# Kernel tuning notes

Hardware: AMD Instinct MI355X
Metric: run time of the kernel (lower is better)

The kernel has to match this reference:

```python
import jax, jax.numpy as jnp
import numpy as np

B, S, E, H, C = 32, 256, 768, 512, 30
IN0 = E + 2  # LSTM layer-0 input size (770)


def _lstm_dir(x_sbf, Wih, Whh, bih, bhh, reverse):
    """One LSTM direction. x_sbf: [S,B,F]. PyTorch gate order i,f,g,o. Returns [S,B,H]."""
    h0 = jnp.zeros((x_sbf.shape[1], Whh.shape[1]), x_sbf.dtype)
    c0 = jnp.zeros_like(h0)
    xW = jnp.einsum('sbf,gf->sbg', x_sbf, Wih) + (bih + bhh)  # precompute input proj

    def step(carry, xw_t):
        h, c = carry
        gates = xw_t + h @ Whh.T
        i, f, g, o = jnp.split(gates, 4, axis=-1)
        c = jax.nn.sigmoid(f) * c + jax.nn.sigmoid(i) * jnp.tanh(g)
        h = jax.nn.sigmoid(o) * jnp.tanh(c)
        return (h, c), h

    _, ys = jax.lax.scan(step, (h0, c0), xW, reverse=reverse)
    return ys  # aligned with input time order


def _bilstm_layer(x_sbf, Wf, Uf, bif, bhf, Wb, Ub, bib, bhb):
    hf = _lstm_dir(x_sbf, Wf, Uf, bif, bhf, reverse=False)
    hb = _lstm_dir(x_sbf, Wb, Ub, bib, bhb, reverse=True)
    return jnp.concatenate([hf, hb], axis=-1)  # [S,B,2H]


def setup_inputs() -> dict:
    key = jax.random.key(0)
    ks = jax.random.split(key, 24)
    d = {
        'hidden_states': jax.random.normal(ks[0], (4, B, S, E), jnp.float32),
        'roles': jax.random.randint(ks[1], (B, S), 0, C),
        'predicates': jax.random.randint(ks[2], (B, S), 0, 2),
    }
    G = 4 * H
    shapes = {
        'Wih_l0f': (G, IN0), 'Whh_l0f': (G, H), 'bih_l0f': (G,), 'bhh_l0f': (G,),
        'Wih_l0b': (G, IN0), 'Whh_l0b': (G, H), 'bih_l0b': (G,), 'bhh_l0b': (G,),
        'Wih_l1f': (G, 2 * H), 'Whh_l1f': (G, H), 'bih_l1f': (G,), 'bhh_l1f': (G,),
        'Wih_l1b': (G, 2 * H), 'Whh_l1b': (G, H), 'bih_l1b': (G,), 'bhh_l1b': (G,),
        'W_out': (C, 2 * H), 'b_out': (C,),
    }
    for i, (name, shp) in enumerate(shapes.items()):
        d[name] = jax.random.normal(ks[3 + i], shp, jnp.float32) * 0.05
    return d


def reference(hidden_states, roles, predicates,
              Wih_l0f, Whh_l0f, bih_l0f, bhh_l0f,
              Wih_l0b, Whh_l0b, bih_l0b, bhh_l0b,
              Wih_l1f, Whh_l1f, bih_l1f, bhh_l1f,
              Wih_l1b, Whh_l1b, bih_l1b, bhh_l1b,
              W_out, b_out):
    # mean of last-4 transformer hidden states: [B,S,E]
    out = hidden_states.mean(axis=0)
    # vectorized predicate-relative features (replaces the Python .item() loops)
    idx_pred = jnp.argmax(predicates, axis=-1)                      # [B]
    mean_word = out.mean(axis=-1)                                   # [B,S]
    mean_pred = jnp.take_along_axis(mean_word, idx_pred[:, None], axis=1)  # [B,1]
    delta = mean_word - mean_pred                                   # [B,S]
    role_mask = ((roles != 0) & (roles != -100)).astype(out.dtype)  # [B,S]
    x = jnp.concatenate([out, delta[..., None], role_mask[..., None]], axis=-1)  # [B,S,E+2]

    # 2-layer BiLSTM (eval mode; inter-layer dropout inactive)
    x = jnp.swapaxes(x, 0, 1)  # [S,B,F]
    x = _bilstm_layer(x, Wih_l0f, Whh_l0f, bih_l0f, bhh_l0f,
                      Wih_l0b, Whh_l0b, bih_l0b, bhh_l0b)
    x = _bilstm_layer(x, Wih_l1f, Whh_l1f, bih_l1f, bhh_l1f,
                      Wih_l1b, Whh_l1b, bih_l1b, bhh_l1b)
    x = jnp.swapaxes(x, 0, 1)  # [B,S,2H]
    return x @ W_out.T + b_out  # [B,S,classes]
```

## Files before the change

### kernel.cpp

```cpp
#include <hip/hip_runtime.h>
#include <hip/hip_bf16.h>
#include <math.h>

#define BB 32
#define SS 256
#define EE 768
#define HH 512
#define GG 2048
#define NCLS 30
#define NWG 16

typedef __attribute__((ext_vector_type(8))) short bf16x8;
typedef __attribute__((ext_vector_type(4))) float f32x4;
typedef unsigned long long u64;

__device__ inline unsigned short f2bf(float f) {
  union { float f; unsigned int u; } v; v.f = f;
  unsigned int r = v.u + 0x7fffu + ((v.u >> 16) & 1u);
  return (unsigned short)(r >> 16);
}
__device__ inline float bf2f(unsigned short u) {
  union { unsigned int u; float f; } v; v.u = ((unsigned int)u) << 16;
  return v.f;
}
__device__ inline float sigm(float x) { return 1.f / (1.f + expf(-x)); }

__device__ inline void load_lds16(const void* g, void* l) {
  __builtin_amdgcn_global_load_lds(
      (const __attribute__((address_space(1))) void*)g,
      (__attribute__((address_space(3))) void*)l, 16, 0, 0);
}

__device__ inline u64 aload64(const u64* p) {
  return __hip_atomic_load(p, __ATOMIC_RELAXED, __HIP_MEMORY_SCOPE_AGENT);
}
__device__ inline void astore64(u64* p, u64 v) {
  __hip_atomic_store(p, v, __ATOMIC_RELAXED, __HIP_MEMORY_SCOPE_AGENT);
}
__device__ inline int aload32(const int* p) {
  return __hip_atomic_load(p, __ATOMIC_RELAXED, __HIP_MEMORY_SCOPE_AGENT);
}
__device__ inline void astore32(int* p, int v) {
  __hip_atomic_store(p, v, __ATOMIC_RELAXED, __HIP_MEMORY_SCOPE_AGENT);
}
__device__ inline void wait_vm0() {
  asm volatile("s_waitcnt vmcnt(0)" ::: "memory");
}

__global__ void k_convpad(const float* __restrict__ src, unsigned short* __restrict__ dst,
                          int R, int Ks, int Kd) {
  int n = R * Kd;
  for (int i = blockIdx.x * blockDim.x + threadIdx.x; i < n; i += gridDim.x * blockDim.x) {
    int r = i / Kd, k = i - r * Kd;
    dst[i] = (k < Ks) ? f2bf(src[(size_t)r * Ks + k]) : (unsigned short)0;
  }
}

__global__ void k_biassum(const float* __restrict__ a, const float* __restrict__ b,
                          float* __restrict__ o) {
  int i = blockIdx.x * 256 + threadIdx.x;
  if (i < GG) o[i] = a[i] + b[i];
}

__global__ void k_meanword(const float* __restrict__ hs, float* __restrict__ mw) {
  int blk = blockIdx.x;
  int b = blk >> 8, s = blk & 255;
  __shared__ float red[256];
  size_t base = ((size_t)b * SS + s) * EE;
  const size_t LSTR = (size_t)BB * SS * EE;
  float acc = 0.f;
  for (int l = 0; l < 4; l++)
    for (int e = threadIdx.x; e < EE; e += 256) acc += hs[l * LSTR + base + e];
  red[threadIdx.x] = acc;
  __syncthreads();
  for (int s2 = 128; s2 > 0; s2 >>= 1) {
    if (threadIdx.x < s2) red[threadIdx.x] += red[threadIdx.x + s2];
    __syncthreads();
  }
  if (threadIdx.x == 0) mw[blk] = red[0] * (1.f / 3072.f);
}

__global__ void k_idxpred(const int* __restrict__ pred, int* __restrict__ idxp) {
  int b = blockIdx.x, l = threadIdx.x;
  const int* pb = pred + b * SS;
  int4 v = *(const int4*)(pb + l * 4);
  int loc = 0x7fffffff;
  if (v.w == 1) loc = 4 * l + 3;
  if (v.z == 1) loc = 4 * l + 2;
  if (v.y == 1) loc = 4 * l + 1;
  if (v.x == 1) loc = 4 * l + 0;
  for (int off = 32; off > 0; off >>= 1) {
    int o = __shfl_down(loc, off);
    loc = min(loc, o);
  }
  if (l == 0) idxp[b] = (loc == 0x7fffffff) ? 0 : loc;
}

__global__ void k_buildA0(const float* __restrict__ hs, const float* __restrict__ mw,
                          const int* __restrict__ idxp, const int* __restrict__ roles,
                          unsigned short* __restrict__ A0) {
  int blk = blockIdx.x;
  int s = blk >> 5, b = blk & 31;
  unsigned short* row = A0 + (size_t)blk * 800;
  size_t base = ((size_t)b * SS + s) * EE;
  const size_t LSTR = (size_t)BB * SS * EE;
  for (int k = threadIdx.x; k < EE; k += 256) {
    float v = hs[base + k] + hs[base + LSTR + k] + hs[base + 2 * LSTR + k] + hs[base + 3 * LSTR + k];
    row[k] = f2bf(v * 0.25f);
  }
  if (threadIdx.x == 0) {
    float d = mw[b * SS + s] - mw[b * SS + idxp[b]];
    row[768] = f2bf(d);
    int rl = roles[b * SS + s];
    row[769] = f2bf((rl != 0 && rl != -100) ? 1.f : 0.f);
  }
  if (threadIdx.x < 30) row[770 + threadIdx.x] = 0;
}

__global__ __launch_bounds__(256) void k_gemm_bt(const unsigned short* __restrict__ A,
                                                 const unsigned short* __restrict__ W,
                                                 const float* __restrict__ bias,
                                                 float* __restrict__ C, int K) {
  __shared__ unsigned short As[128 * 32];
  __shared__ unsigned short Bs[128 * 32];
  const int tid = threadIdx.x;
  const int wave = tid >> 6, lane = tid & 63;
  const int l15 = lane & 15, quad = lane >> 4;
  const int m0 = blockIdx.y * 128, n0 = blockIdx.x * 128;
  const int wr = (wave >> 1) * 64, wc = (wave & 1) * 64;
  const int srow = wave * 16 + (lane >> 2);
  const int scol = (lane & 3) * 8;

  f32x4 acc[4][4];
#pragma unroll
  for (int i = 0; i < 4; i++)
#pragma unroll
    for (int j = 0; j < 4; j++) acc[i][j] = (f32x4){0.f, 0.f, 0.f, 0.f};

  for (int k0 = 0; k0 < K; k0 += 32) {
#pragma unroll
    for (int rep = 0; rep < 2; rep++) {
      load_lds16(A + (size_t)(m0 + rep * 64 + srow) * K + k0 + scol,
                 &As[(rep * 64 + wave * 16) * 32]);
      load_lds16(W + (size_t)(n0 + rep * 64 + srow) * K + k0 + scol,
                 &Bs[(rep * 64 + wave * 16) * 32]);
    }
    __syncthreads();
    bf16x8 af[4], bfr[4];
#pragma unroll
    for (int i = 0; i < 4; i++) af[i] = *(const bf16x8*)&As[(wr + i * 16 + l15) * 32 + quad * 8];
#pragma unroll
    for (int j = 0; j < 4; j++) bfr[j] = *(const bf16x8*)&Bs[(wc + j * 16 + l15) * 32 + quad * 8];
#pragma unroll
    for (int i = 0; i < 4; i++)
#pragma unroll
      for (int j = 0; j < 4; j++)
        acc[i][j] = __builtin_amdgcn_mfma_f32_16x16x32_bf16(af[i], bfr[j], acc[i][j], 0, 0, 0);
    __syncthreads();
  }

#pragma unroll
  for (int j = 0; j < 4; j++) {
    int n = n0 + wc + j * 16 + l15;
    float bv = bias[n];
#pragma unroll
    for (int i = 0; i < 4; i++) {
      int m = m0 + wr + i * 16 + quad * 4;
      int s = m >> 5, b = m & 31;
      f32x4 v = acc[i][j];
      f32x4 outv = {v[0] + bv, v[1] + bv, v[2] + bv, v[3] + bv};
      *(f32x4*)(C + ((size_t)s * GG + n) * BB + b) = outv;
    }
  }
}

__global__ __launch_bounds__(256, 1) void k_recurrent(const float* __restrict__ xWf,
                                                      const float* __restrict__ xWb,
                                                      const unsigned short* __restrict__ WhhF,
                                                      const unsigned short* __restrict__ WhhB,
                                                      u64* __restrict__ hbuf,
                                                      unsigned short* __restrict__ Hout,
                                                      int* __restrict__ flags) {
  const int wg = blockIdx.x, dir = wg >> 4, slice = wg & 15;
  const int tid = threadIdx.x, wave = tid >> 6, lane = tid & 63;
  const int l15 = lane & 15, quad = lane >> 4;
  const int u0 = slice * 32;
  const unsigned short* Whh = dir ? WhhB : WhhF;
  const float* xW = dir ? xWb : xWf;
  u64* hbT = hbuf + (size_t)dir * 8192;
  int* flg = flags + dir * (NWG * 32);

  __shared__ __attribute__((aligned(16))) short hlds[32][528];
  __shared__ float gbuf[4][32][32];

  for (int i = tid; i < 32 * 264; i += 256) ((unsigned int*)hlds)[i] = 0;

  bf16x8 bfrag[2][16];
#pragma unroll
  for (int j = 0; j < 2; j++) {
    const unsigned short* wrow = Whh + (size_t)(wave * HH + u0 + j * 16 + l15) * HH + quad * 8;
#pragma unroll
    for (int kk = 0; kk < 16; kk++) bfrag[j][kk] = *(const bf16x8*)(wrow + kk * 32);
  }

  const int cb = tid >> 3;
  const int cu = (tid & 7) * 4;
  float cst[4] = {0.f, 0.f, 0.f, 0.f};

  f32x4 xv[2][2];
  {
    const int time0 = dir ? (SS - 1) : 0;
#pragma unroll
    for (int j = 0; j < 2; j++)
#pragma unroll
      for (int i = 0; i < 2; i++)
        xv[i][j] = *(const f32x4*)(xW + ((size_t)time0 * GG + wave * HH + u0 + j * 16 + l15) * BB +
                                   i * 16 + quad * 4);
  }
  __syncthreads();

  for (int t = 0; t < SS; t++) {
    const int time = dir ? (SS - 1 - t) : t;

    f32x4 acc[2][2];
#pragma unroll
    for (int i = 0; i < 2; i++)
#pragma unroll
      for (int j = 0; j < 2; j++) acc[i][j] = xv[i][j];

#pragma unroll
    for (int kk = 0; kk < 16; kk++) {
      bf16x8 a0 = *(const bf16x8*)&hlds[l15][quad * 8 + kk * 32];
      bf16x8 a1 = *(const bf16x8*)&hlds[16 + l15][quad * 8 + kk * 32];
      acc[0][0] = __builtin_amdgcn_mfma_f32_16x16x32_bf16(a0, bfrag[0][kk], acc[0][0], 0, 0, 0);
      acc[0][1] = __builtin_amdgcn_mfma_f32_16x16x32_bf16(a0, bfrag[1][kk], acc[0][1], 0, 0, 0);
      acc[1][0] = __builtin_amdgcn_mfma_f32_16x16x32_bf16(a1, bfrag[0][kk], acc[1][0], 0, 0, 0);
      acc[1][1] = __builtin_amdgcn_mfma_f32_16x16x32_bf16(a1, bfrag[1][kk], acc[1][1], 0, 0, 0);
    }
#pragma unroll
    for (int i = 0; i < 2; i++)
#pragma unroll
      for (int j = 0; j < 2; j++)
#pragma unroll
        for (int r = 0; r < 4; r++)
          gbuf[wave][i * 16 + quad * 4 + r][j * 16 + l15] = acc[i][j][r];
    __syncthreads();

    f32x4 G0 = *(const f32x4*)&gbuf[0][cb][cu];
    f32x4 G1 = *(const f32x4*)&gbuf[1][cb][cu];
    f32x4 G2 = *(const f32x4*)&gbuf[2][cb][cu];
    f32x4 G3 = *(const f32x4*)&gbuf[3][cb][cu];
    unsigned short hs4[4];
#pragma unroll
    for (int q = 0; q < 4; q++) {
      float gi = sigm(G0[q]), gf = sigm(G1[q]), gg = tanhf(G2[q]), go = sigm(G3[q]);
      cst[q] = gf * cst[q] + gi * gg;
      hs4[q] = f2bf(go * tanhf(cst[q]));
    }
    const u64 packed =
        (u64)((unsigned)hs4[0] | ((unsigned)hs4[1] << 16)) |
        ((u64)((unsigned)hs4[2] | ((unsigned)hs4[3] << 16)) << 32);

    const int slw = (t + 1) & 1;
    astore64(hbT + slw * 4096 + (cb * 128 + ((u0 + cu) >> 2)), packed);
    wait_vm0();
    __syncthreads();
    if (tid == 0) astore32(&flg[slice * 32], t + 1);

    *(uint2*)(Hout + ((size_t)time * BB + cb) * 1024 + dir * HH + u0 + cu) =
        make_uint2((unsigned)packed, (unsigned)(packed >> 32));
    {
      const int tn = (t + 1 < SS) ? (t + 1) : t;
      const int timen = dir ? (SS - 1 - tn) : tn;
#pragma unroll
      for (int j = 0; j < 2; j++)
#pragma unroll
        for (int i = 0; i < 2; i++)
          xv[i][j] = *(const f32x4*)(xW + ((size_t)timen * GG + wave * HH + u0 + j * 16 + l15) * BB +
                                     i * 16 + quad * 4);
    }

    if (t + 1 < SS) {
      const int need = t + 1;
      if (wave == 0) {
        for (;;) {
          int v = (lane < NWG) ? aload32(&flg[lane * 32]) : need;
          if (__all(v >= need)) break;
        }
      }
      __syncthreads();

      const u64* src = hbT + slw * 4096;
      u64 v[16];
#pragma unroll
      for (int i = 0; i < 16; i++) v[i] = aload64(src + tid + i * 256);
#pragma unroll
      for (int i = 0; i < 16; i++) {
        const int g = tid + i * 256;
        *(u64*)&hlds[g >> 7][(g & 127) * 4] = v[i];
      }
    }
    __syncthreads();
  }
}

__global__ __launch_bounds__(256) void k_out(const unsigned short* __restrict__ H1,
                                             const float* __restrict__ Wout,
                                             const float* __restrict__ bout,
                                             float* __restrict__ out) {
  __shared__ float rows[8][1024];
  __shared__ float ps[8][32][8];
  const int rb = blockIdx.x * 8;
  const int tid = threadIdx.x;
  for (int idx = tid; idx < 8 * 1024; idx += 256) {
    int r = idx >> 10, k = idx & 1023;
    rows[r][k] = bf2f(H1[(size_t)(rb + r) * 1024 + k]);
  }
  __syncthreads();
  const int c = tid & 31, p = tid >> 5;
  float acc[8] = {0.f, 0.f, 0.f, 0.f, 0.f, 0.f, 0.f, 0.f};
  if (c < NCLS) {
    const float* wr = Wout + (size_t)c * 1024 + p * 128;
    for (int k = 0; k < 128; k++) {
      float w = wr[k];
#pragma unroll
      for (int r = 0; r < 8; r++) acc[r] += rows[r][p * 128 + k] * w;
    }
  }
#pragma unroll
  for (int r = 0; r < 8; r++) ps[p][c][r] = acc[r];
  __syncthreads();
  if (p == 0 && c < NCLS) {
    for (int r = 0; r < 8; r++) {
      float v = bout[c];
#pragma unroll
      for (int q = 0; q < 8; q++) v += ps[q][c][r];
      int row = rb + r, s = row >> 5, b = row & 31;
      out[((size_t)b * SS + s) * NCLS + c] = v;
    }
  }
}

extern "C" void kernel_launch(void* const* d_in, const int* in_sizes, int n_in,
                              void* d_out, int out_size, void* d_ws, size_t ws_size,
                              hipStream_t stream) {
  const float* hs     = (const float*)d_in[0];
  const int*   roles  = (const int*)d_in[1];
  const int*   preds  = (const int*)d_in[2];
  const float* Wih0f  = (const float*)d_in[3];
  const float* Whh0f  = (const float*)d_in[4];
  const float* bih0f  = (const float*)d_in[5];
  const float* bhh0f  = (const float*)d_in[6];
  const float* Wih0b  = (const float*)d_in[7];
  const float* Whh0b  = (const float*)d_in[8];
  const float* bih0b  = (const float*)d_in[9];
  const float* bhh0b  = (const float*)d_in[10];
  const float* Wih1f  = (const float*)d_in[11];
  const float* Whh1f  = (const float*)d_in[12];
  const float* bih1f  = (const float*)d_in[13];
  const float* bhh1f  = (const float*)d_in[14];
  const float* Wih1b  = (const float*)d_in[15];
  const float* Whh1b  = (const float*)d_in[16];
  const float* bih1b  = (const float*)d_in[17];
  const float* bhh1b  = (const float*)d_in[18];
  const float* Wout   = (const float*)d_in[19];
  const float* bout   = (const float*)d_in[20];
  (void)in_sizes; (void)n_in; (void)out_size; (void)ws_size;

  char* ws = (char*)d_ws;
  size_t off = 0;
  auto alloc = [&](size_t bytes) -> char* {
    char* p = ws + off;
    off += (bytes + 255) & ~(size_t)255;
    return p;
  };
  float* xWf = (float*)alloc((size_t)SS * GG * BB * 4);
  float* xWb = (float*)alloc((size_t)SS * GG * BB * 4);
  unsigned short* A0  = (unsigned short*)alloc((size_t)8192 * 800 * 2);
  unsigned short* H0p = (unsigned short*)alloc((size_t)8192 * 1024 * 2);
  unsigned short* H1p = (unsigned short*)alloc((size_t)8192 * 1024 * 2);
  unsigned short* Wb0f = (unsigned short*)alloc((size_t)GG * 800 * 2);
  unsigned short* Wb0b = (unsigned short*)alloc((size_t)GG * 800 * 2);
  unsigned short* Wb1f = (unsigned short*)alloc((size_t)GG * 1024 * 2);
  unsigned short* Wb1b = (unsigned short*)alloc((size_t)GG * 1024 * 2);
  unsigned short* Wh0f = (unsigned short*)alloc((size_t)GG * HH * 2);
  unsigned short* Wh0b = (unsigned short*)alloc((size_t)GG * HH * 2);
  unsigned short* Wh1f = (unsigned short*)alloc((size_t)GG * HH * 2);
  unsigned short* Wh1b = (unsigned short*)alloc((size_t)GG * HH * 2);
  float* bsum = (float*)alloc(4 * GG * 4);
  float* mw   = (float*)alloc((size_t)BB * SS * 4);
  int*   idxp = (int*)alloc(256);
  u64* hbuf0 = (u64*)alloc(131072);
  u64* hbuf1 = (u64*)alloc(131072);
  char* zbase = alloc(8192);
  int* flags0 = (int*)zbase;
  int* flags1 = (int*)(zbase + 4096);

  hipMemsetAsync(zbase, 0, 8192, stream);

  k_convpad<<<1024, 256, 0, stream>>>(Wih0f, Wb0f, GG, 770, 800);
  k_convpad<<<1024, 256, 0, stream>>>(Wih0b, Wb0b, GG, 770, 800);
  k_convpad<<<1024, 256, 0, stream>>>(Wih1f, Wb1f, GG, 1024, 1024);
  k_convpad<<<1024, 256, 0, stream>>>(Wih1b, Wb1b, GG, 1024, 1024);
  k_convpad<<<1024, 256, 0, stream>>>(Whh0f, Wh0f, GG, 512, 512);
  k_convpad<<<1024, 256, 0, stream>>>(Whh0b, Wh0b, GG, 512, 512);
  k_convpad<<<1024, 256, 0, stream>>>(Whh1f, Wh1f, GG, 512, 512);
  k_convpad<<<1024, 256, 0, stream>>>(Whh1b, Wh1b, GG, 512, 512);
  k_biassum<<<8, 256, 0, stream>>>(bih0f, bhh0f, bsum);
  k_biassum<<<8, 256, 0, stream>>>(bih0b, bhh0b, bsum + 2048);
  k_biassum<<<8, 256, 0, stream>>>(bih1f, bhh1f, bsum + 4096);
  k_biassum<<<8, 256, 0, stream>>>(bih1b, bhh1b, bsum + 6144);

  k_meanword<<<BB * SS, 256, 0, stream>>>(hs, mw);
  k_idxpred<<<BB, 64, 0, stream>>>(preds, idxp);
  k_buildA0<<<BB * SS, 256, 0, stream>>>(hs, mw, idxp, roles, A0);

  dim3 gg(16, 64);
  k_gemm_bt<<<gg, 256, 0, stream>>>(A0, Wb0f, bsum, xWf, 800);
  k_gemm_bt<<<gg, 256, 0, stream>>>(A0, Wb0b, bsum + 2048, xWb, 800);
  k_recurrent<<<2 * NWG, 256, 0, stream>>>(xWf, xWb, Wh0f, Wh0b, hbuf0, H0p, flags0);
  k_gemm_bt<<<gg, 256, 0, stream>>>(H0p, Wb1f, bsum + 4096, xWf, 1024);
  k_gemm_bt<<<gg, 256, 0, stream>>>(H0p, Wb1b, bsum + 6144, xWb, 1024);
  k_recurrent<<<2 * NWG, 256, 0, stream>>>(xWf, xWb, Wh1f, Wh1b, hbuf1, H1p, flags1);
  k_out<<<1024, 256, 0, stream>>>(H1p, Wout, bout, (float*)d_out);
}
```

Baseline: 2.798 ms.

## Replace flag-based step barrier with parity bits embedded in h values

The recurrent kernel stops publishing per-workgroup completion flags after a vmcnt wait and barrier. Instead, the low mantissa bit of each bf16 hidden value carries a step-parity tag, and consumers spin on the h data itself until every tag matches. The workgroup's own slice is written straight to LDS. This removes one store-then-flag round trip and a barrier per timestep, at the cost of one bit of bf16 precision in h. Separately, the mean-word reduction is fused into A0 construction, which removes an extra full pass over hidden_states; a small kernel then fills in the predicate-delta column.

After: 2.807 ms. No clear change (+0.3%).

```diff
diff --git a/kernel.cpp b/kernel.cpp
--- a/kernel.cpp
+++ b/kernel.cpp
@@ -37,15 +37,6 @@
 __device__ inline void astore64(u64* p, u64 v) {
   __hip_atomic_store(p, v, __ATOMIC_RELAXED, __HIP_MEMORY_SCOPE_AGENT);
 }
-__device__ inline int aload32(const int* p) {
-  return __hip_atomic_load(p, __ATOMIC_RELAXED, __HIP_MEMORY_SCOPE_AGENT);
-}
-__device__ inline void astore32(int* p, int v) {
-  __hip_atomic_store(p, v, __ATOMIC_RELAXED, __HIP_MEMORY_SCOPE_AGENT);
-}
-__device__ inline void wait_vm0() {
-  asm volatile("s_waitcnt vmcnt(0)" ::: "memory");
-}
 
 __global__ void k_convpad(const float* __restrict__ src, unsigned short* __restrict__ dst,
                           int R, int Ks, int Kd) {
@@ -62,22 +53,13 @@
   if (i < GG) o[i] = a[i] + b[i];
 }
 
-__global__ void k_meanword(const float* __restrict__ hs, float* __restrict__ mw) {
-  int blk = blockIdx.x;
-  int b = blk >> 8, s = blk & 255;
-  __shared__ float red[256];
-  size_t base = ((size_t)b * SS + s) * EE;
-  const size_t LSTR = (size_t)BB * SS * EE;
-  float acc = 0.f;
-  for (int l = 0; l < 4; l++)
-    for (int e = threadIdx.x; e < EE; e += 256) acc += hs[l * LSTR + base + e];
-  red[threadIdx.x] = acc;
-  __syncthreads();
-  for (int s2 = 128; s2 > 0; s2 >>= 1) {
-    if (threadIdx.x < s2) red[threadIdx.x] += red[threadIdx.x + s2];
-    __syncthreads();
-  }
-  if (threadIdx.x == 0) mw[blk] = red[0] * (1.f / 3072.f);
+__global__ void k_hinit(u64* __restrict__ h0, u64* __restrict__ h1) {
+  int i = blockIdx.x * 256 + threadIdx.x;
+  if (i < 16384) {
+    u64 v = ((i >> 12) & 1) ? 0x0001000100010001ULL : 0ULL;
+    h0[i] = v;
+    h1[i] = v;
+  }
 }
 
 __global__ void k_idxpred(const int* __restrict__ pred, int* __restrict__ idxp) {
@@ -96,25 +78,41 @@
   if (l == 0) idxp[b] = (loc == 0x7fffffff) ? 0 : loc;
 }
 
-__global__ void k_buildA0(const float* __restrict__ hs, const float* __restrict__ mw,
-                          const int* __restrict__ idxp, const int* __restrict__ roles,
-                          unsigned short* __restrict__ A0) {
+__global__ void k_buildA0(const float* __restrict__ hs, const int* __restrict__ roles,
+                          float* __restrict__ mw, unsigned short* __restrict__ A0) {
   int blk = blockIdx.x;
   int s = blk >> 5, b = blk & 31;
   unsigned short* row = A0 + (size_t)blk * 800;
   size_t base = ((size_t)b * SS + s) * EE;
   const size_t LSTR = (size_t)BB * SS * EE;
+  __shared__ float red[256];
+  float part = 0.f;
   for (int k = threadIdx.x; k < EE; k += 256) {
-    float v = hs[base + k] + hs[base + LSTR + k] + hs[base + 2 * LSTR + k] + hs[base + 3 * LSTR + k];
-    row[k] = f2bf(v * 0.25f);
-  }
-  if (threadIdx.x == 0) {
-    float d = mw[b * SS + s] - mw[b * SS + idxp[b]];
-    row[768] = f2bf(d);
+    float v = (hs[base + k] + hs[base + LSTR + k] + hs[base + 2 * LSTR + k] +
+               hs[base + 3 * LSTR + k]) * 0.25f;
+    part += v;
+    row[k] = f2bf(v);
+  }
+  red[threadIdx.x] = part;
+  __syncthreads();
+  for (int s2 = 128; s2 > 0; s2 >>= 1) {
+    if (threadIdx.x < s2) red[threadIdx.x] += red[threadIdx.x + s2];
+    __syncthreads();
+  }
+  if (threadIdx.x == 0) mw[b * SS + s] = red[0] * (1.f / 768.f);
+  if (threadIdx.x == 1) {
     int rl = roles[b * SS + s];
     row[769] = f2bf((rl != 0 && rl != -100) ? 1.f : 0.f);
   }
   if (threadIdx.x < 30) row[770 + threadIdx.x] = 0;
+}
+
+__global__ void k_predfeat(const float* __restrict__ mw, const int* __restrict__ idxp,
+                           unsigned short* __restrict__ A0) {
+  int i = blockIdx.x * 256 + threadIdx.x;
+  int b = i >> 8, s = i & 255;
+  float d = mw[i] - mw[b * SS + idxp[b]];
+  A0[(size_t)(s * 32 + b) * 800 + 768] = f2bf(d);
 }
 
 __global__ __launch_bounds__(256) void k_gemm_bt(const unsigned short* __restrict__ A,
@@ -179,8 +177,7 @@
                                                       const unsigned short* __restrict__ WhhF,
                                                       const unsigned short* __restrict__ WhhB,
                                                       u64* __restrict__ hbuf,
-                                                      unsigned short* __restrict__ Hout,
-                                                      int* __restrict__ flags) {
+                                                      unsigned short* __restrict__ Hout) {
   const int wg = blockIdx.x, dir = wg >> 4, slice = wg & 15;
   const int tid = threadIdx.x, wave = tid >> 6, lane = tid & 63;
   const int l15 = lane & 15, quad = lane >> 4;
@@ -188,7 +185,6 @@
   const unsigned short* Whh = dir ? WhhB : WhhF;
   const float* xW = dir ? xWb : xWf;
   u64* hbT = hbuf + (size_t)dir * 8192;
-  int* flg = flags + dir * (NWG * 32);
 
   __shared__ __attribute__((aligned(16))) short hlds[32][528];
   __shared__ float gbuf[4][32][32];
@@ -206,6 +202,10 @@
   const int cb = tid >> 3;
   const int cu = (tid & 7) * 4;
   float cst[4] = {0.f, 0.f, 0.f, 0.f};
+
+  const int guc = tid & 127;
+  const int bb0 = tid >> 7;
+  const bool ownCol = ((guc >> 3) == slice);
 
   f32x4 xv[2][2];
   {
@@ -250,12 +250,13 @@
     f32x4 G1 = *(const f32x4*)&gbuf[1][cb][cu];
     f32x4 G2 = *(const f32x4*)&gbuf[2][cb][cu];
     f32x4 G3 = *(const f32x4*)&gbuf[3][cb][cu];
+    const unsigned Tb = ((unsigned)(t + 1) >> 1) & 1u;
     unsigned short hs4[4];
 #pragma unroll
     for (int q = 0; q < 4; q++) {
       float gi = sigm(G0[q]), gf = sigm(G1[q]), gg = tanhf(G2[q]), go = sigm(G3[q]);
       cst[q] = gf * cst[q] + gi * gg;
-      hs4[q] = f2bf(go * tanhf(cst[q]));
+      hs4[q] = (unsigned short)((f2bf(go * tanhf(cst[q])) & 0xFFFEu) | Tb);
     }
     const u64 packed =
         (u64)((unsigned)hs4[0] | ((unsigned)hs4[1] << 16)) |
@@ -263,9 +264,7 @@
 
     const int slw = (t + 1) & 1;
     astore64(hbT + slw * 4096 + (cb * 128 + ((u0 + cu) >> 2)), packed);
-    wait_vm0();
-    __syncthreads();
-    if (tid == 0) astore32(&flg[slice * 32], t + 1);
+    *(u64*)&hlds[cb][u0 + cu] = packed;
 
     *(uint2*)(Hout + ((size_t)time * BB + cb) * 1024 + dir * HH + u0 + cu) =
         make_uint2((unsigned)packed, (unsigned)(packed >> 32));
@@ -280,25 +279,25 @@
                                      i * 16 + quad * 4);
     }
 
-    if (t + 1 < SS) {
-      const int need = t + 1;
-      if (wave == 0) {
-        for (;;) {
-          int v = (lane < NWG) ? aload32(&flg[lane * 32]) : need;
-          if (__all(v >= need)) break;
-        }
-      }
-      __syncthreads();
-
+    if (t + 1 < SS && !ownCol) {
+      const u64 tmask = 0x0001000100010001ULL;
+      const u64 tpat = Tb ? tmask : 0ULL;
       const u64* src = hbT + slw * 4096;
       u64 v[16];
 #pragma unroll
-      for (int i = 0; i < 16; i++) v[i] = aload64(src + tid + i * 256);
-#pragma unroll
-      for (int i = 0; i < 16; i++) {
-        const int g = tid + i * 256;
-        *(u64*)&hlds[g >> 7][(g & 127) * 4] = v[i];
+      for (int i = 0; i < 16; i++) v[i] = aload64(src + (bb0 + 2 * i) * 128 + guc);
+      for (;;) {
+        unsigned st = 0;
+#pragma unroll
+        for (int i = 0; i < 16; i++)
+          if (((v[i] ^ tpat) & tmask) != 0ULL) st |= 1u << i;
+        if (!__any(st)) break;
+#pragma unroll
+        for (int i = 0; i < 16; i++)
+          if (st & (1u << i)) v[i] = aload64(src + (bb0 + 2 * i) * 128 + guc);
       }
+#pragma unroll
+      for (int i = 0; i < 16; i++) *(u64*)&hlds[bb0 + 2 * i][guc * 4] = v[i];
     }
     __syncthreads();
   }
@@ -392,11 +391,8 @@
   int*   idxp = (int*)alloc(256);
   u64* hbuf0 = (u64*)alloc(131072);
   u64* hbuf1 = (u64*)alloc(131072);
-  char* zbase = alloc(8192);
-  int* flags0 = (int*)zbase;
-  int* flags1 = (int*)(zbase + 4096);
-
-  hipMemsetAsync(zbase, 0, 8192, stream);
+
+  k_hinit<<<64, 256, 0, stream>>>(hbuf0, hbuf1);
 
   k_convpad<<<1024, 256, 0, stream>>>(Wih0f, Wb0f, GG, 770, 800);
   k_convpad<<<1024, 256, 0, stream>>>(Wih0b, Wb0b, GG, 770, 800);
@@ -411,16 +407,16 @@
   k_biassum<<<8, 256, 0, stream>>>(bih1f, bhh1f, bsum + 4096);
   k_biassum<<<8, 256, 0, stream>>>(bih1b, bhh1b, bsum + 6144);
 
-  k_meanword<<<BB * SS, 256, 0, stream>>>(hs, mw);
+  k_buildA0<<<BB * SS, 256, 0, stream>>>(hs, roles, mw, A0);
   k_idxpred<<<BB, 64, 0, stream>>>(preds, idxp);
-  k_buildA0<<<BB * SS, 256, 0, stream>>>(hs, mw, idxp, roles, A0);
+  k_predfeat<<<32, 256, 0, stream>>>(mw, idxp, A0);
 
   dim3 gg(16, 64);
   k_gemm_bt<<<gg, 256, 0, stream>>>(A0, Wb0f, bsum, xWf, 800);
   k_gemm_bt<<<gg, 256, 0, stream>>>(A0, Wb0b, bsum + 2048, xWb, 800);
-  k_recurrent<<<2 * NWG, 256, 0, stream>>>(xWf, xWb, Wh0f, Wh0b, hbuf0, H0p, flags0);
+  k_recurrent<<<2 * NWG, 256, 0, stream>>>(xWf, xWb, Wh0f, Wh0b, hbuf0, H0p);
   k_gemm_bt<<<gg, 256, 0, stream>>>(H0p, Wb1f, bsum + 4096, xWf, 1024);
   k_gemm_bt<<<gg, 256, 0, stream>>>(H0p, Wb1b, bsum + 6144, xWb, 1024);
-  k_recurrent<<<2 * NWG, 256, 0, stream>>>(xWf, xWb, Wh1f, Wh1b, hbuf1, H1p, flags1);
+  k_recurrent<<<2 * NWG, 256, 0, stream>>>(xWf, xWb, Wh1f, Wh1b, hbuf1, H1p);
   k_out<<<1024, 256, 0, stream>>>(H1p, Wout, bout, (float*)d_out);
 }
```
